# Performance work log

Measured on AMD Instinct MI355X. Metric: run time of the kernel, lower is better.

## Reference

```python
import jax, jax.numpy as jnp
import numpy as np

SEQ, D_IN, D_OUT = 8192, 768, 128


def setup_inputs() -> dict:
    key = jax.random.key(0)
    k1, k2, k3, k4 = jax.random.split(key, 4)
    x = jax.random.normal(k1, (SEQ, D_IN), dtype=jnp.float32)
    # torch nn.Linear weights are stored as [d_out, d_in]
    scale = 1.0 / np.sqrt(D_IN)
    w_query = jax.random.normal(k2, (D_OUT, D_IN), dtype=jnp.float32) * scale
    w_key = jax.random.normal(k3, (D_OUT, D_IN), dtype=jnp.float32) * scale
    w_value = jax.random.normal(k4, (D_OUT, D_IN), dtype=jnp.float32) * scale
    return {"x": x, "w_query": w_query, "w_key": w_key, "w_value": w_value}


def reference(x, w_query, w_key, w_value):
    # Linear with bias=False: y = x @ W.T   (W is [d_out, d_in])
    q = x @ w_query.T                      # [N, d_out]
    k = x @ w_key.T                        # [N, d_out]
    v = x @ w_value.T                      # [N, d_out]
    inv_sqrt_d = 1.0 / jnp.sqrt(jnp.float32(k.shape[-1]))
    scores = (q @ k.T) * inv_sqrt_d        # [N, N] -- fully materialized, as in source
    weights = jax.nn.softmax(scores, axis=-1)
    return weights @ v                     # [N, d_out]
```

## Files before the change

### kernel.cpp

```cpp
#include <hip/hip_runtime.h>
#include <stdint.h>

#define SEQ 8192
#define DIN 768
#define DOUT 128

typedef __attribute__((ext_vector_type(8))) short short8;
typedef __attribute__((ext_vector_type(8))) unsigned short ushort8v;
typedef __attribute__((ext_vector_type(4))) float f32x4;

#define CEXPF (1.4426950408889634f * 0.08838834764831845f)

#if __has_builtin(__builtin_amdgcn_exp2f)
#define EXP2(x) __builtin_amdgcn_exp2f(x)
#else
#define EXP2(x) __builtin_exp2f(x)
#endif

__device__ __forceinline__ unsigned short f2bf(float f) {
  return (unsigned short)((__float_as_uint(f) + 0x8000u) >> 16);
}

__device__ __forceinline__ void gload_lds16(const void* g, void* l) {
  __builtin_amdgcn_global_load_lds(
      (const __attribute__((address_space(1))) void*)g,
      (__attribute__((address_space(3))) void*)l, 16, 0, 0);
}

__global__ void wconv_kernel(const float* __restrict__ wq,
                             const float* __restrict__ wk,
                             const float* __restrict__ wv,
                             unsigned short* __restrict__ Wb) {
  int idx4 = (blockIdx.x * 256 + threadIdx.x) * 4;
  int z = idx4 / (DOUT * DIN);
  int rem = idx4 - z * (DOUT * DIN);
  const float* src = (z == 0) ? wq : (z == 1) ? wk : wv;
  float4 v = *(const float4*)(src + rem);
  float sc = (z == 0) ? CEXPF : 1.0f;
  ushort4 o;
  o.x = f2bf(v.x * sc); o.y = f2bf(v.y * sc);
  o.z = f2bf(v.z * sc); o.w = f2bf(v.w * sc);
  *(ushort4*)(Wb + idx4) = o;
}

__launch_bounds__(256, 3)
__global__ void qkv_kernel(const float* __restrict__ x,
                           const unsigned short* __restrict__ Wb,
                           unsigned short* __restrict__ Qb,
                           unsigned short* __restrict__ Kb,
                           unsigned short* __restrict__ Vtb) {
  __shared__ unsigned short smem[4352];
  unsigned short* xs = smem;

  const int t    = threadIdx.x;
  const int w    = t >> 6;
  const int lane = t & 63;
  const int g    = lane >> 4;
  const int r    = lane & 15;
  const int z    = blockIdx.y;
  const int m0   = blockIdx.x * 32;
  const unsigned short* Wz = Wb + (size_t)z * DOUT * DIN;

  f32x4 acc[2][2];
#pragma unroll
  for (int i = 0; i < 2; i++)
#pragma unroll
    for (int j = 0; j < 2; j++) acc[i][j] = 0.f;

  const int srow = t >> 3;
  const int scol = (t & 7) * 4;

#pragma unroll 1
  for (int kb = 0; kb < DIN; kb += 32) {
    short8 af[2];
#pragma unroll
    for (int mt = 0; mt < 2; mt++)
      af[mt] = *(const short8*)(Wz + (size_t)(w * 32 + mt * 16 + r) * DIN + kb + g * 8);
    float4 xv = *(const float4*)(x + (size_t)(m0 + srow) * DIN + kb + scol);
    ushort4 xb;
    xb.x = f2bf(xv.x); xb.y = f2bf(xv.y); xb.z = f2bf(xv.z); xb.w = f2bf(xv.w);
    *(ushort4*)&xs[srow * 40 + scol] = xb;
    __syncthreads();
    short8 bf[2];
#pragma unroll
    for (int nt = 0; nt < 2; nt++)
      bf[nt] = *(const short8*)&xs[(nt * 16 + r) * 40 + g * 8];
#pragma unroll
    for (int mt = 0; mt < 2; mt++)
#pragma unroll
      for (int nt = 0; nt < 2; nt++)
        acc[mt][nt] = __builtin_amdgcn_mfma_f32_16x16x32_bf16(af[mt], bf[nt], acc[mt][nt], 0, 0, 0);
    __syncthreads();
  }

  if (z < 2) {
    unsigned short* out = (z == 0) ? Qb : Kb;
#pragma unroll
    for (int mt = 0; mt < 2; mt++)
#pragma unroll
      for (int nt = 0; nt < 2; nt++) {
        ushort4 o;
        o.x = f2bf(acc[mt][nt][0]); o.y = f2bf(acc[mt][nt][1]);
        o.z = f2bf(acc[mt][nt][2]); o.w = f2bf(acc[mt][nt][3]);
        *(ushort4*)(out + (size_t)(m0 + nt * 16 + r) * DOUT + w * 32 + mt * 16 + g * 4) = o;
      }
  } else {
    unsigned short* ct = smem;
#pragma unroll
    for (int mt = 0; mt < 2; mt++)
#pragma unroll
      for (int nt = 0; nt < 2; nt++) {
        ushort4 o;
        o.x = f2bf(acc[mt][nt][0]); o.y = f2bf(acc[mt][nt][1]);
        o.z = f2bf(acc[mt][nt][2]); o.w = f2bf(acc[mt][nt][3]);
        *(ushort4*)&ct[(nt * 16 + r) * 136 + w * 32 + mt * 16 + g * 4] = o;
      }
    __syncthreads();
    int col  = t >> 1;
    int half = (t & 1) * 16;
#pragma unroll
    for (int h2 = 0; h2 < 2; h2++) {
      ushort8v a;
#pragma unroll
      for (int i = 0; i < 8; i++) a[i] = ct[(half + h2 * 8 + i) * 136 + col];
      *(ushort8v*)(Vtb + (size_t)col * SEQ + m0 + half + h2 * 8) = a;
    }
  }
}

__launch_bounds__(256, 2)
__global__ void attn_kernel(const unsigned short* __restrict__ Qb,
                            const unsigned short* __restrict__ Kb,
                            const unsigned short* __restrict__ Vtb,
                            float* __restrict__ Opart,
                            float* __restrict__ lpart) {
  __shared__ unsigned char lds[51200];
  unsigned char* Kl = lds;
  unsigned char* Vl = lds + 16384;

  const int t    = threadIdx.x;
  const int wave = t >> 6;
  const int lane = t & 63;
  const int g    = lane >> 4;
  const int r    = lane & 15;
  unsigned short* Pl = (unsigned short*)(lds + 32768 + wave * 4608);

  const int qb = blockIdx.x;
  const int sp = blockIdx.y;
  const int q0 = qb * 128 + wave * 32;

  short8 qf[2][4];
#pragma unroll
  for (int nt = 0; nt < 2; nt++)
#pragma unroll
    for (int kc = 0; kc < 4; kc++)
      qf[nt][kc] = *(const short8*)(Qb + (size_t)(q0 + nt * 16 + r) * DOUT + kc * 32 + g * 8);

  short8 onesf;
#pragma unroll
  for (int j = 0; j < 8; j++) onesf[j] = (r == 0) ? (short)0x3F80 : (short)0;

  f32x4 oacc[2][8];
  f32x4 lacc[2];
#pragma unroll
  for (int st = 0; st < 2; st++) {
    lacc[st] = 0.f;
#pragma unroll
    for (int n = 0; n < 8; n++) oacc[st][n] = 0.f;
  }

#pragma unroll 1
  for (int it = 0; it < 16; it++) {
    const int kv0 = sp * 1024 + it * 64;
#pragma unroll
    for (int c = 0; c < 4; c++) {
      int idx = (wave * 4 + c) * 64 + lane;
      int krow = idx >> 4, kch = idx & 15;
      gload_lds16(Kb + ((size_t)(kv0 + krow) << 7) + ((kch ^ (krow & 15)) << 3),
                  Kl + ((wave * 4 + c) << 10) + (lane << 4));
      int d = idx >> 3, c2 = idx & 7;
      gload_lds16(Vtb + (size_t)d * SEQ + kv0 + ((c2 ^ (d & 7)) << 3),
                  Vl + ((wave * 4 + c) << 10) + (lane << 4));
    }
    __syncthreads();

    f32x4 sf[4][2];
#pragma unroll
    for (int mt = 0; mt < 4; mt++)
#pragma unroll
      for (int nt = 0; nt < 2; nt++) sf[mt][nt] = 0.f;
#pragma unroll
    for (int mt = 0; mt < 4; mt++) {
      int row = mt * 16 + r;
#pragma unroll
      for (int kc = 0; kc < 4; kc++) {
        short8 kf = *(const short8*)(Kl + row * 256 + (((kc * 4 + g) ^ (row & 15)) << 4));
        sf[mt][0] = __builtin_amdgcn_mfma_f32_16x16x32_bf16(kf, qf[0][kc], sf[mt][0], 0, 0, 0);
        sf[mt][1] = __builtin_amdgcn_mfma_f32_16x16x32_bf16(kf, qf[1][kc], sf[mt][1], 0, 0, 0);
      }
    }

#pragma unroll
    for (int mt = 0; mt < 4; mt++)
#pragma unroll
      for (int nt = 0; nt < 2; nt++) {
        ushort4 p;
        p.x = f2bf(EXP2(sf[mt][nt][0]));
        p.y = f2bf(EXP2(sf[mt][nt][1]));
        p.z = f2bf(EXP2(sf[mt][nt][2]));
        p.w = f2bf(EXP2(sf[mt][nt][3]));
        *(ushort4*)(Pl + (nt * 16 + r) * 72 + mt * 16 + g * 4) = p;
      }
    short8 pf[2][2];
#pragma unroll
    for (int st = 0; st < 2; st++)
#pragma unroll
      for (int c2 = 0; c2 < 2; c2++)
        pf[st][c2] = *(const short8*)(Pl + (st * 16 + r) * 72 + c2 * 32 + g * 8);

#pragma unroll
    for (int nt = 0; nt < 8; nt++) {
      int d = nt * 16 + r;
#pragma unroll
      for (int c2 = 0; c2 < 2; c2++) {
        short8 vf = *(const short8*)(Vl + d * 128 + (((c2 * 4 + g) ^ (d & 7)) << 4));
        oacc[0][nt] = __builtin_amdgcn_mfma_f32_16x16x32_bf16(pf[0][c2], vf, oacc[0][nt], 0, 0, 0);
        oacc[1][nt] = __builtin_amdgcn_mfma_f32_16x16x32_bf16(pf[1][c2], vf, oacc[1][nt], 0, 0, 0);
      }
    }
#pragma unroll
    for (int st = 0; st < 2; st++) {
      lacc[st] = __builtin_amdgcn_mfma_f32_16x16x32_bf16(pf[st][0], onesf, lacc[st], 0, 0, 0);
      lacc[st] = __builtin_amdgcn_mfma_f32_16x16x32_bf16(pf[st][1], onesf, lacc[st], 0, 0, 0);
    }
    __syncthreads();
  }

  const size_t pbase = (size_t)sp * SEQ;
#pragma unroll
  for (int st = 0; st < 2; st++)
#pragma unroll
    for (int rr = 0; rr < 4; rr++) {
      int qrow = q0 + st * 16 + g * 4 + rr;
#pragma unroll
      for (int nt = 0; nt < 8; nt++)
        Opart[(pbase + qrow) * DOUT + nt * 16 + r] = oacc[st][nt][rr];
      if (r == 0) lpart[pbase + qrow] = lacc[st][rr];
    }
}

__global__ void combine_kernel(const float* __restrict__ Opart,
                               const float* __restrict__ lpart,
                               float* __restrict__ out) {
  int idx = blockIdx.x * 256 + threadIdx.x;
  int s   = idx >> 5;
  int d4  = (idx & 31) * 4;
  float L = 0.f;
  f32x4 acc = 0.f;
#pragma unroll
  for (int p = 0; p < 8; p++) {
    L += lpart[p * SEQ + s];
    acc += *(const f32x4*)(Opart + ((size_t)p * SEQ + s) * DOUT + d4);
  }
  f32x4 res = acc * (1.0f / L);
  *(f32x4*)(out + (size_t)s * DOUT + d4) = res;
}

extern "C" void kernel_launch(void* const* d_in, const int* in_sizes, int n_in,
                              void* d_out, int out_size, void* d_ws, size_t ws_size,
                              hipStream_t stream) {
  const float* x  = (const float*)d_in[0];
  const float* wq = (const float*)d_in[1];
  const float* wk = (const float*)d_in[2];
  const float* wv = (const float*)d_in[3];
  float* out = (float*)d_out;

  unsigned short* Qb  = (unsigned short*)d_ws;
  unsigned short* Kb  = Qb + (size_t)SEQ * DOUT;
  unsigned short* Vtb = Kb + (size_t)SEQ * DOUT;
  float* Opart = (float*)(Vtb + (size_t)SEQ * DOUT);
  float* lpart = Opart + (size_t)8 * SEQ * DOUT;
  unsigned short* Wb  = (unsigned short*)Opart;
  if (ws_size < (size_t)(6291456 + 33554432 + 262144)) return;

  wconv_kernel<<<dim3(288), 256, 0, stream>>>(wq, wk, wv, Wb);
  qkv_kernel<<<dim3(256, 3), 256, 0, stream>>>(x, Wb, Qb, Kb, Vtb);
  attn_kernel<<<dim3(64, 8), 256, 0, stream>>>(Qb, Kb, Vtb, Opart, lpart);
  combine_kernel<<<dim3(1024), 256, 0, stream>>>(Opart, lpart, out);
}
```

Before: 140.7 us.

## Overlap K/V tile loads with MFMA compute and drop LDS staging in QKV projection

The attention kernel now issues the next K tile load right after the QK^T phase and the next V tile load right after the PV phase, using manual vmcnt waits and barriers so memory traffic overlaps compute instead of a load-sync-compute loop. MFMA sections are raised in priority with s_setprio. The QKV projection kernel now reads x directly from global into registers and converts to bf16 there, removing the LDS staging and its two barriers per k-step, and unrolls that loop by two. The cost is more redundant global reads of x and fragile hand-placed waitcnt and barrier synchronisation.

```diff
diff --git a/kernel.cpp b/kernel.cpp
--- a/kernel.cpp
+++ b/kernel.cpp
@@ -50,7 +50,6 @@
                            unsigned short* __restrict__ Kb,
                            unsigned short* __restrict__ Vtb) {
   __shared__ unsigned short smem[4352];
-  unsigned short* xs = smem;
 
   const int t    = threadIdx.x;
   const int w    = t >> 6;
@@ -67,30 +66,30 @@
 #pragma unroll
     for (int j = 0; j < 2; j++) acc[i][j] = 0.f;
 
-  const int srow = t >> 3;
-  const int scol = (t & 7) * 4;
-
-#pragma unroll 1
+#pragma unroll 2
   for (int kb = 0; kb < DIN; kb += 32) {
     short8 af[2];
 #pragma unroll
     for (int mt = 0; mt < 2; mt++)
       af[mt] = *(const short8*)(Wz + (size_t)(w * 32 + mt * 16 + r) * DIN + kb + g * 8);
-    float4 xv = *(const float4*)(x + (size_t)(m0 + srow) * DIN + kb + scol);
-    ushort4 xb;
-    xb.x = f2bf(xv.x); xb.y = f2bf(xv.y); xb.z = f2bf(xv.z); xb.w = f2bf(xv.w);
-    *(ushort4*)&xs[srow * 40 + scol] = xb;
-    __syncthreads();
     short8 bf[2];
 #pragma unroll
-    for (int nt = 0; nt < 2; nt++)
-      bf[nt] = *(const short8*)&xs[(nt * 16 + r) * 40 + g * 8];
+    for (int nt = 0; nt < 2; nt++) {
+      const float* xp = x + (size_t)(m0 + nt * 16 + r) * DIN + kb + g * 8;
+      float4 lo = *(const float4*)xp;
+      float4 hi = *(const float4*)(xp + 4);
+      short8 b;
+      b[0] = (short)f2bf(lo.x); b[1] = (short)f2bf(lo.y);
+      b[2] = (short)f2bf(lo.z); b[3] = (short)f2bf(lo.w);
+      b[4] = (short)f2bf(hi.x); b[5] = (short)f2bf(hi.y);
+      b[6] = (short)f2bf(hi.z); b[7] = (short)f2bf(hi.w);
+      bf[nt] = b;
+    }
 #pragma unroll
     for (int mt = 0; mt < 2; mt++)
 #pragma unroll
       for (int nt = 0; nt < 2; nt++)
         acc[mt][nt] = __builtin_amdgcn_mfma_f32_16x16x32_bf16(af[mt], bf[nt], acc[mt][nt], 0, 0, 0);
-    __syncthreads();
   }
 
   if (z < 2) {
@@ -148,47 +147,61 @@
   const int qb = blockIdx.x;
   const int sp = blockIdx.y;
   const int q0 = qb * 128 + wave * 32;
-
-  short8 qf[2][4];
-#pragma unroll
-  for (int nt = 0; nt < 2; nt++)
-#pragma unroll
-    for (int kc = 0; kc < 4; kc++)
-      qf[nt][kc] = *(const short8*)(Qb + (size_t)(q0 + nt * 16 + r) * DOUT + kc * 32 + g * 8);
-
-  short8 onesf;
-#pragma unroll
-  for (int j = 0; j < 8; j++) onesf[j] = (r == 0) ? (short)0x3F80 : (short)0;
-
-  f32x4 oacc[2][8];
-  f32x4 lacc[2];
-#pragma unroll
-  for (int st = 0; st < 2; st++) {
-    lacc[st] = 0.f;
-#pragma unroll
-    for (int n = 0; n < 8; n++) oacc[st][n] = 0.f;
-  }
-
-#pragma unroll 1
-  for (int it = 0; it < 16; it++) {
-    const int kv0 = sp * 1024 + it * 64;
+  const int kvbase = sp * 1024;
+
+  auto stageK = [&](int kv0) {
 #pragma unroll
     for (int c = 0; c < 4; c++) {
       int idx = (wave * 4 + c) * 64 + lane;
       int krow = idx >> 4, kch = idx & 15;
       gload_lds16(Kb + ((size_t)(kv0 + krow) << 7) + ((kch ^ (krow & 15)) << 3),
                   Kl + ((wave * 4 + c) << 10) + (lane << 4));
+    }
+  };
+  auto stageV = [&](int kv0) {
+#pragma unroll
+    for (int c = 0; c < 4; c++) {
+      int idx = (wave * 4 + c) * 64 + lane;
       int d = idx >> 3, c2 = idx & 7;
       gload_lds16(Vtb + (size_t)d * SEQ + kv0 + ((c2 ^ (d & 7)) << 3),
                   Vl + ((wave * 4 + c) << 10) + (lane << 4));
     }
-    __syncthreads();
-
+  };
+
+  short8 qf[2][4];
+#pragma unroll
+  for (int nt = 0; nt < 2; nt++)
+#pragma unroll
+    for (int kc = 0; kc < 4; kc++)
+      qf[nt][kc] = *(const short8*)(Qb + (size_t)(q0 + nt * 16 + r) * DOUT + kc * 32 + g * 8);
+
+  short8 onesf;
+#pragma unroll
+  for (int j = 0; j < 8; j++) onesf[j] = (r == 0) ? (short)0x3F80 : (short)0;
+
+  f32x4 oacc[2][8];
+  f32x4 lacc[2];
+#pragma unroll
+  for (int st = 0; st < 2; st++) {
+    lacc[st] = 0.f;
+#pragma unroll
+    for (int n = 0; n < 8; n++) oacc[st][n] = 0.f;
+  }
+
+  stageK(kvbase);
+  stageV(kvbase);
+  asm volatile("s_waitcnt vmcnt(0)" ::: "memory");
+  __builtin_amdgcn_s_barrier();
+  asm volatile("" ::: "memory");
+
+#pragma unroll 1
+  for (int it = 0; it < 16; it++) {
     f32x4 sf[4][2];
 #pragma unroll
     for (int mt = 0; mt < 4; mt++)
 #pragma unroll
       for (int nt = 0; nt < 2; nt++) sf[mt][nt] = 0.f;
+    __builtin_amdgcn_s_setprio(1);
 #pragma unroll
     for (int mt = 0; mt < 4; mt++) {
       int row = mt * 16 + r;
@@ -199,6 +212,7 @@
         sf[mt][1] = __builtin_amdgcn_mfma_f32_16x16x32_bf16(kf, qf[1][kc], sf[mt][1], 0, 0, 0);
       }
     }
+    __builtin_amdgcn_s_setprio(0);
 
 #pragma unroll
     for (int mt = 0; mt < 4; mt++)
@@ -218,6 +232,12 @@
       for (int c2 = 0; c2 < 2; c2++)
         pf[st][c2] = *(const short8*)(Pl + (st * 16 + r) * 72 + c2 * 32 + g * 8);
 
+    asm volatile("s_waitcnt vmcnt(0)" ::: "memory");
+    __builtin_amdgcn_s_barrier();
+    asm volatile("" ::: "memory");
+    if (it < 15) stageK(kvbase + (it + 1) * 64);
+
+    __builtin_amdgcn_s_setprio(1);
 #pragma unroll
     for (int nt = 0; nt < 8; nt++) {
       int d = nt * 16 + r;
@@ -233,7 +253,17 @@
       lacc[st] = __builtin_amdgcn_mfma_f32_16x16x32_bf16(pf[st][0], onesf, lacc[st], 0, 0, 0);
       lacc[st] = __builtin_amdgcn_mfma_f32_16x16x32_bf16(pf[st][1], onesf, lacc[st], 0, 0, 0);
     }
-    __syncthreads();
+    __builtin_amdgcn_s_setprio(0);
+
+    asm volatile("" ::: "memory");
+    __builtin_amdgcn_s_barrier();
+    asm volatile("" ::: "memory");
+    if (it < 15) {
+      stageV(kvbase + (it + 1) * 64);
+      asm volatile("s_waitcnt vmcnt(4)" ::: "memory");
+      __builtin_amdgcn_s_barrier();
+      asm volatile("" ::: "memory");
+    }
   }
 
   const size_t pbase = (size_t)sp * SEQ;
```

After: 165.7 us. +17.7%, slower.
